# Optimization experiments

Measured on AMD Instinct MI355X. Metric: run time of the kernel, lower is better.

The kernel has to match this reference:

```python
import jax, jax.numpy as jnp
import numpy as np

B, N = 32, 512


def _stick_breaking(b, x_mask):
    """Row-major stick-breaking recurrence, O(N^2) sequential steps.

    Equivalent to the TF while_loop: for step in range(N*N), m=step//N, n=step%N:
      fut      = max(0, x_mask[:,m,n+1:] - sum_{m'<m} x[:,m',n+1:])  (col partial sums)
      mfm      = sum_j fut_j
      row_sum  = sum_{n'<n} x[:,m,n']
      col_sum  = sum_{m'<m} x[:,m',n]
      lower    = mask[m,n]*max(0, 1 - row_sum - mfm)
      upper    = mask[m,n]*min(1 - row_sum, 1 - col_sum)
      x[m,n]   = lower + b[m,n]*(upper - lower)
    Key insight: during row m the column partial sums are constant, so the
    future-mass terms for every n can be precomputed as an exclusive reverse
    cumsum; only the within-row dependency (row_sum) needs a scan.
    """
    Bb, Nn, _ = b.shape
    dt = b.dtype

    def row_step(col_sums, inputs):
        b_row, mask_row = inputs                      # [B, N] each
        fut = jnp.maximum(0.0, mask_row - col_sums)   # [B, N]
        # mfm[:, n] = sum_{j > n} fut[:, j]  (exclusive reverse cumsum)
        mfm = jnp.flip(jnp.cumsum(jnp.flip(fut, -1), axis=-1), -1) - fut

        def col_step(row_sum, inp):
            b_mn, m_mn, mfm_n, cs_n = inp             # [B] each
            lower = m_mn * jnp.maximum(0.0, 1.0 - row_sum - mfm_n)
            upper = m_mn * jnp.minimum(1.0 - row_sum, 1.0 - cs_n)
            p = lower + b_mn * (upper - lower)
            return row_sum + p, p

        _, row = jax.lax.scan(
            col_step,
            jnp.zeros((Bb,), dt),
            (b_row.T, mask_row.T, mfm.T, col_sums.T),
        )
        row = row.T                                   # [B, N]
        return col_sums + row, row

    _, rows = jax.lax.scan(
        row_step,
        jnp.zeros((Bb, Nn), dt),
        (jnp.swapaxes(b, 0, 1), jnp.swapaxes(x_mask, 0, 1)),
    )
    return jnp.swapaxes(rows, 0, 1)                   # [B, N, N]


def setup_inputs() -> dict:
    key = jax.random.key(0)
    k1, _ = jax.random.split(key)
    x = jax.random.normal(k1, (B, N, N), dtype=jnp.float32)
    x_mask = jnp.ones((B, N, N), dtype=jnp.float32)
    return {"x": x, "x_mask": x_mask}


def reference(x, x_mask):
    # layer.call applies sigmoid to the logits before stick-breaking
    return _stick_breaking(jax.nn.sigmoid(x), x_mask)
```

## Files before the change

kernel.cpp:

```cpp
#include <hip/hip_runtime.h>

#define NBATCH 32
#define NDIM 512
#define NFAST 448
#define NQUAD 112
#define NWAVE 8


__device__ __forceinline__ float prefix_inc(float x) {
  asm("s_nop 1\n\t"
      "v_add_f32_dpp %0, %0, %0 row_shr:1 row_mask:0xf bank_mask:0xf\n\t"
      "s_nop 1\n\t"
      "v_add_f32_dpp %0, %0, %0 row_shr:2 row_mask:0xf bank_mask:0xf\n\t"
      "s_nop 1\n\t"
      "v_add_f32_dpp %0, %0, %0 row_shr:4 row_mask:0xf bank_mask:0xf\n\t"
      "s_nop 1\n\t"
      "v_add_f32_dpp %0, %0, %0 row_shr:8 row_mask:0xf bank_mask:0xf\n\t"
      "s_nop 1\n\t"
      "v_add_f32_dpp %0, %0, %0 row_bcast:15 row_mask:0xa bank_mask:0xf\n\t"
      "s_nop 1\n\t"
      "v_add_f32_dpp %0, %0, %0 row_bcast:31 row_mask:0xc bank_mask:0xf\n\t"
      "s_nop 1"
      : "+v"(x));
  return x;
}

__device__ __forceinline__ void prefix_inc2(float& a, float& b) {
  asm("s_nop 1\n\t"
      "v_add_f32_dpp %0, %0, %0 row_shr:1 row_mask:0xf bank_mask:0xf\n\t"
      "v_add_f32_dpp %1, %1, %1 row_shr:1 row_mask:0xf bank_mask:0xf\n\t"
      "s_nop 0\n\t"
      "v_add_f32_dpp %0, %0, %0 row_shr:2 row_mask:0xf bank_mask:0xf\n\t"
      "v_add_f32_dpp %1, %1, %1 row_shr:2 row_mask:0xf bank_mask:0xf\n\t"
      "s_nop 0\n\t"
      "v_add_f32_dpp %0, %0, %0 row_shr:4 row_mask:0xf bank_mask:0xf\n\t"
      "v_add_f32_dpp %1, %1, %1 row_shr:4 row_mask:0xf bank_mask:0xf\n\t"
      "s_nop 0\n\t"
      "v_add_f32_dpp %0, %0, %0 row_shr:8 row_mask:0xf bank_mask:0xf\n\t"
      "v_add_f32_dpp %1, %1, %1 row_shr:8 row_mask:0xf bank_mask:0xf\n\t"
      "s_nop 0\n\t"
      "v_add_f32_dpp %0, %0, %0 row_bcast:15 row_mask:0xa bank_mask:0xf\n\t"
      "v_add_f32_dpp %1, %1, %1 row_bcast:15 row_mask:0xa bank_mask:0xf\n\t"
      "s_nop 0\n\t"
      "v_add_f32_dpp %0, %0, %0 row_bcast:31 row_mask:0xc bank_mask:0xf\n\t"
      "v_add_f32_dpp %1, %1, %1 row_bcast:31 row_mask:0xc bank_mask:0xf\n\t"
      "s_nop 1"
      : "+v"(a), "+v"(b));
}

__device__ __forceinline__ void aff_scan(float& A, float& B) {
  asm("s_nop 1\n\t"
      "v_fmac_f32_dpp %1, %1, %0 row_shr:1 row_mask:0xf bank_mask:0xf\n\t"
      "v_mul_f32_dpp  %0, %0, %0 row_shr:1 row_mask:0xf bank_mask:0xf\n\t"
      "s_nop 0\n\t"
      "v_fmac_f32_dpp %1, %1, %0 row_shr:2 row_mask:0xf bank_mask:0xf\n\t"
      "v_mul_f32_dpp  %0, %0, %0 row_shr:2 row_mask:0xf bank_mask:0xf\n\t"
      "s_nop 0\n\t"
      "v_fmac_f32_dpp %1, %1, %0 row_shr:4 row_mask:0xf bank_mask:0xf\n\t"
      "v_mul_f32_dpp  %0, %0, %0 row_shr:4 row_mask:0xf bank_mask:0xf\n\t"
      "s_nop 0\n\t"
      "v_fmac_f32_dpp %1, %1, %0 row_shr:8 row_mask:0xf bank_mask:0xf\n\t"
      "v_mul_f32_dpp  %0, %0, %0 row_shr:8 row_mask:0xf bank_mask:0xf\n\t"
      "s_nop 0\n\t"
      "v_fmac_f32_dpp %1, %1, %0 row_bcast:15 row_mask:0xa bank_mask:0xf\n\t"
      "v_mul_f32_dpp  %0, %0, %0 row_bcast:15 row_mask:0xa bank_mask:0xf\n\t"
      "s_nop 0\n\t"
      "v_fmac_f32_dpp %1, %1, %0 row_bcast:31 row_mask:0xc bank_mask:0xf\n\t"
      "v_mul_f32_dpp  %0, %0, %0 row_bcast:31 row_mask:0xc bank_mask:0xf\n\t"
      "s_nop 1"
      : "+v"(A), "+v"(B));
}

__device__ __forceinline__ float wave_shr1(float x, float fill) {
  return __int_as_float(__builtin_amdgcn_update_dpp(
      __float_as_int(fill), __float_as_int(x), 0x138 , 0xf, 0xf,
      false));
}

__device__ __forceinline__ void wg_barrier() {
  asm volatile("s_waitcnt lgkmcnt(0)" ::: "memory");
  __builtin_amdgcn_s_barrier();
  asm volatile("" ::: "memory");
}

__global__ __launch_bounds__(512, 2)
void sb_kernel(const float* __restrict__ x, const float* __restrict__ xm,
               float* __restrict__ out) {
  const int tid = (int)threadIdx.x;
  const int lane = tid & 63;
  const int w = __builtin_amdgcn_readfirstlane(tid >> 6);
  const int w2 = 2 * w;
  const size_t base =
      (size_t)blockIdx.x * NDIM * NDIM + (size_t)(w * 64 + lane);
  const float* xb = x + base;
  const float* mb = xm + base;
  float* ob = out + base;

  __shared__ float4 recs[NFAST];
  __shared__ alignas(16) float ex_sa[NWAVE];
  __shared__ alignas(16) float ex_S[NWAVE];
  __shared__ alignas(16) float ex_A[NWAVE];
  __shared__ alignas(16) float ex_B[NWAVE];

  float w8, t8;
  float c2_0, oc2_0, c2_1, oc2_1, c2_2, oc2_2, c2_3, oc2_3;
  float c1, c2, oc2;
  float fu = 0.0f, S = 0.0f;

  float X0 = xb[0], X1 = xb[NDIM], X2 = xb[2 * NDIM], X3 = xb[3 * NDIM];
  float M0 = mb[0], M1 = mb[NDIM], M2 = mb[2 * NDIM], M3 = mb[3 * NDIM];
  float Bx0 = xb[4 * NDIM], Bx1 = xb[5 * NDIM], Bx2 = xb[6 * NDIM],
        Bx3 = xb[7 * NDIM];
  float Bm0 = mb[4 * NDIM], Bm1 = mb[5 * NDIM], Bm2 = mb[6 * NDIM],
        Bm3 = mb[7 * NDIM];
  float Ax0 = Bx0, Ax1 = Bx1, Ax2 = Bx2, Ax3 = Bx3;
  float Am0 = Bm0, Am1 = Bm1, Am2 = Bm2, Am3 = Bm3;

  {
    float s0 = __builtin_amdgcn_rcpf(1.0f + __expf(-X0));
    float s1 = __builtin_amdgcn_rcpf(1.0f + __expf(-X1));
    float s2 = __builtin_amdgcn_rcpf(1.0f + __expf(-X2));
    float s3 = __builtin_amdgcn_rcpf(1.0f + __expf(-X3));
    c2_0 = M0 * s0;
    oc2_0 = 1.0f - c2_0;
    c2_1 = M1 * s1;
    oc2_1 = 1.0f - c2_1;
    c2_2 = M2 * s2;
    oc2_2 = 1.0f - c2_2;
    c2_3 = M3 * s3;
    oc2_3 = 1.0f - c2_3;
    w8 = 1.0f;
    t8 = c2_0;
  }

  const float* px = xb + (long)(8 - 8 * w) * NDIM;
  const float* pm = mb + (long)(8 - 8 * w) * NDIM;
  float* po = ob - (long)(8 * w) * NDIM;

  auto row_fast = [&](int m, const float4& r, float c2r, float oc2r,
                      float* pO) {
    float PA = prefix_inc(t8);
    float uin = fmaxf(1.0f - (r.z + (PA - t8)), 0.0f);
    bool pW = w8 < uin;
    float A = pW ? 1.0f : oc2r;
    float Bv = pW ? (-t8) : 0.0f;
    aff_scan(A, Bv);
    float Aex = wave_shr1(A, 1.0f);
    float Bex = wave_shr1(Bv, 0.0f);
    if (w < NWAVE - 1 && lane == 63)
      recs[m] = make_float4(A * r.x, fmaf(A, r.y, Bv), r.z + PA, 0.0f);
    float E = r.x + r.y;
    float e = fminf(fmaxf(fmaf(Aex, E, Bex), 0.0f), 1.0f);
    float p = c2r * fminf(e, w8);
    w8 -= p;
    *pO = p;
  };

  auto quad_step = [&](int t, int k, float& WX0, float& WX1, float& WX2,
                       float& WX3, float& WM0, float& WM1, float& WM2,
                       float& WM3, const float& RX0, const float& RX1,
                       const float& RX2, const float& RX3, const float& RM0,
                       const float& RM1, const float& RM2, const float& RM3) {
    const int q = t - w2;
    if ((unsigned)q < (unsigned)NQUAD) {
      const int m = 4 * q;
      float4 r0 = make_float4(1.0f, 0.0f, 0.0f, 0.0f);
      float4 r1 = r0, r2 = r0, r3 = r0;
      if (w > 0) {
        r0 = recs[m];
        r1 = recs[m + 1];
        r2 = recs[m + 2];
        r3 = recs[m + 3];
      }
      const float* pxk = px + (size_t)(4 * k) * NDIM;
      const float* pmk = pm + (size_t)(4 * k) * NDIM;
      WX0 = pxk[0];
      WX1 = pxk[NDIM];
      WX2 = pxk[2 * NDIM];
      WX3 = pxk[3 * NDIM];
      WM0 = pmk[0];
      WM1 = pmk[NDIM];
      WM2 = pmk[2 * NDIM];
      WM3 = pmk[3 * NDIM];

      float s0 = __builtin_amdgcn_rcpf(1.0f + __expf(-RX0));
      float s1 = __builtin_amdgcn_rcpf(1.0f + __expf(-RX1));
      float s2 = __builtin_amdgcn_rcpf(1.0f + __expf(-RX2));
      float s3 = __builtin_amdgcn_rcpf(1.0f + __expf(-RX3));
      float c2n0 = RM0 * s0, oc2n0 = 1.0f - c2n0;
      float c2n1 = RM1 * s1, oc2n1 = 1.0f - c2n1;
      float c2n2 = RM2 * s2, oc2n2 = 1.0f - c2n2;
      float c2n3 = RM3 * s3, oc2n3 = 1.0f - c2n3;

      float* pok = po + (size_t)(4 * k) * NDIM;
      row_fast(m + 0, r0, c2_0, oc2_0, pok);
      t8 = c2_1 * w8;
      row_fast(m + 1, r1, c2_1, oc2_1, pok + NDIM);
      t8 = c2_2 * w8;
      row_fast(m + 2, r2, c2_2, oc2_2, pok + 2 * NDIM);
      t8 = c2_3 * w8;
      row_fast(m + 3, r3, c2_3, oc2_3, pok + 3 * NDIM);
      t8 = c2n0 * w8;
      c2_0 = c2n0;
      oc2_0 = oc2n0;
      c2_1 = c2n1;
      oc2_1 = oc2n1;
      c2_2 = c2n2;
      oc2_2 = oc2n2;
      c2_3 = c2n3;
      oc2_3 = oc2n3;
    }
  };

#pragma unroll 1
  for (int t = 0; t < NQUAD + 2 * (NWAVE - 1); t += 2) {
    quad_step(t + 0, 0, Ax0, Ax1, Ax2, Ax3, Am0, Am1, Am2, Am3, Bx0, Bx1, Bx2,
              Bx3, Bm0, Bm1, Bm2, Bm3);
    quad_step(t + 1, 1, Bx0, Bx1, Bx2, Bx3, Bm0, Bm1, Bm2, Bm3, Ax0, Ax1, Ax2,
              Ax3, Am0, Am1, Am2, Am3);
    wg_barrier();
    px += 8 * NDIM;
    pm += 8 * NDIM;
    po += 8 * NDIM;
  }

  float fx0, fm0, fx1, fm1, fx2, fm2, fx3, fm3;
  {
    float m448 = mb[(size_t)448 * NDIM];
    fx1 = xb[(size_t)449 * NDIM];
    fm1 = mb[(size_t)449 * NDIM];
    fx2 = xb[(size_t)450 * NDIM];
    fm2 = mb[(size_t)450 * NDIM];
    fx3 = xb[(size_t)451 * NDIM];
    fm3 = mb[(size_t)451 * NDIM];
    fx0 = fx1;
    fm0 = fm1;
    c2 = c2_0;
    oc2 = oc2_0;
    c1 = m448 - c2;
    float om = 1.0f - m448;
    fu = fmaxf(w8 - om, 0.0f);
    S = fu;
  }

  auto row_full = [&](int m, float& WX, float& WM, const float& RX,
                      const float& RM) {
    const size_t nro = (size_t)((m + 4) & (NDIM - 1)) * NDIM;
    WX = xb[nro];
    WM = mb[nro];

    float PS = S, PA = t8;
    prefix_inc2(PS, PA);

    if (lane == 63) {
      ex_sa[w] = PA;
      ex_S[w] = PS;
    }
    wg_barrier();

    float4 sl = *(const float4*)&ex_sa[0];
    float4 sh = *(const float4*)&ex_sa[4];
    float4 Sl = *(const float4*)&ex_S[0];
    float4 Sh = *(const float4*)&ex_S[4];
    float off_sa = 0.0f, off_S = 0.0f;
    if (w > 0) { off_sa += sl.x; off_S += Sl.x; }
    if (w > 1) { off_sa += sl.y; off_S += Sl.y; }
    if (w > 2) { off_sa += sl.z; off_S += Sl.z; }
    if (w > 3) { off_sa += sl.w; off_S += Sl.w; }
    if (w > 4) { off_sa += sh.x; off_S += Sh.x; }
    if (w > 5) { off_sa += sh.y; off_S += Sh.y; }
    if (w > 6) { off_sa += sh.z; off_S += Sh.z; }
    float Tg =
        ((Sl.x + Sl.y) + (Sl.z + Sl.w)) + ((Sh.x + Sh.y) + (Sh.z + Sh.w));

    float uin = fmaxf(1.0f - (off_sa + (PA - t8)), 0.0f);
    float R_ = (Tg - off_S) - PS;
    float nc1m = -c1 * R_;

    bool pW = w8 < uin;
    float aP = pW ? 1.0f : oc2;
    float bP = pW ? (-t8) : 0.0f;
    bool pL = (uin - R_) > 0.0f;
    if (pL) {
      aP -= c1;
      bP -= nc1m;
    }

    float A = aP, Bv = bP;
    aff_scan(A, Bv);
    float Aex = wave_shr1(A, 1.0f);
    float Bex = wave_shr1(Bv, 0.0f);

    if (lane == 63) {
      ex_A[w] = A;
      ex_B[w] = Bv;
    }
    wg_barrier();

    float4 Al = *(const float4*)&ex_A[0];
    float4 Ah = *(const float4*)&ex_A[4];
    float4 Bl = *(const float4*)&ex_B[0];
    float4 Bh = *(const float4*)&ex_B[4];
    float E = 1.0f;
    if (w > 0) E = fmaf(Al.x, E, Bl.x);
    if (w > 1) E = fmaf(Al.y, E, Bl.y);
    if (w > 2) E = fmaf(Al.z, E, Bl.z);
    if (w > 3) E = fmaf(Al.w, E, Bl.w);
    if (w > 4) E = fmaf(Ah.x, E, Bh.x);
    if (w > 5) E = fmaf(Ah.y, E, Bh.y);
    if (w > 6) E = fmaf(Ah.z, E, Bh.z);
    float e = fminf(fmaxf(fmaf(Aex, E, Bex), 0.0f), 1.0f);

    float sg = __builtin_amdgcn_rcpf(1.0f + __expf(-RX));
    float c2n = RM * sg;
    float oc2n = 1.0f - c2n;
    float c1n = RM - c2n;
    float omn = 1.0f - RM;

    float U = fminf(e, w8);
    float g = fmaxf(fmaf(c1, e, nc1m), 0.0f);
    float p = fmaf(c2, U, g);
    w8 -= p;
    ob[(size_t)m * NDIM] = p;

    t8 = c2n * w8;
    fu = fmaxf(w8 - omn, 0.0f);
    S = fu;
    c2 = c2n;
    oc2 = oc2n;
    c1 = c1n;
  };

#pragma unroll 1
  for (int m = NFAST; m < NDIM; m += 4) {
    row_full(m + 0, fx0, fm0, fx1, fm1);
    row_full(m + 1, fx1, fm1, fx2, fm2);
    row_full(m + 2, fx2, fm2, fx3, fm3);
    row_full(m + 3, fx3, fm3, fx0, fm0);
  }
}

extern "C" void kernel_launch(void* const* d_in, const int* in_sizes, int n_in,
                              void* d_out, int out_size, void* d_ws,
                              size_t ws_size, hipStream_t stream) {
  const float* x = (const float*)d_in[0];
  const float* xmask = (const float*)d_in[1];
  float* out = (float*)d_out;
  (void)in_sizes;
  (void)n_in;
  (void)out_size;
  (void)d_ws;
  (void)ws_size;
  hipLaunchKernelGGL(sb_kernel, dim3(NBATCH), dim3(512), 0, stream, x, xmask,
                     out);
}
```

Before: 235.6 us.

## Tighten wave pipeline skew to one quad and hide sigmoid in DPP scan nops

Cuts the skew of the wavefront pipeline across waves from two quads to one and puts a barrier after every quad step instead of every pair, so the loop has fewer fill steps. The sigmoid for the next rows is now computed inside the inline-asm DPP prefix scan, filling the s_nop slots that were previously idle. The cost is twice as many workgroup barriers, plus hand-scheduled asm whose hazard spacing must stay correct for DPP. Prefetch register setup is adjusted to match the new skew.

```diff
diff --git a/kernel.cpp b/kernel.cpp
--- a/kernel.cpp
+++ b/kernel.cpp
@@ -7,22 +7,29 @@
 #define NWAVE 8
 
 
-__device__ __forceinline__ float prefix_inc(float x) {
-  asm("s_nop 1\n\t"
+__device__ __forceinline__ void prefix_prep(float& p, float rx, float rm,
+                                            float& c2n, float& oc2n) {
+  float t0, t1, t2;
+  asm("v_mul_f32 %1, 0xbfb8aa3b, %6\n\t"
+      "s_nop 0\n\t"
       "v_add_f32_dpp %0, %0, %0 row_shr:1 row_mask:0xf bank_mask:0xf\n\t"
-      "s_nop 1\n\t"
+      "v_exp_f32 %1, %1\n\t"
+      "s_nop 0\n\t"
       "v_add_f32_dpp %0, %0, %0 row_shr:2 row_mask:0xf bank_mask:0xf\n\t"
-      "s_nop 1\n\t"
+      "v_add_f32 %2, 1.0, %1\n\t"
+      "s_nop 0\n\t"
       "v_add_f32_dpp %0, %0, %0 row_shr:4 row_mask:0xf bank_mask:0xf\n\t"
-      "s_nop 1\n\t"
+      "v_rcp_f32 %3, %2\n\t"
+      "s_nop 0\n\t"
       "v_add_f32_dpp %0, %0, %0 row_shr:8 row_mask:0xf bank_mask:0xf\n\t"
-      "s_nop 1\n\t"
+      "v_mul_f32 %4, %7, %3\n\t"
+      "s_nop 0\n\t"
       "v_add_f32_dpp %0, %0, %0 row_bcast:15 row_mask:0xa bank_mask:0xf\n\t"
-      "s_nop 1\n\t"
-      "v_add_f32_dpp %0, %0, %0 row_bcast:31 row_mask:0xc bank_mask:0xf\n\t"
-      "s_nop 1"
-      : "+v"(x));
-  return x;
+      "v_sub_f32 %5, 1.0, %4\n\t"
+      "s_nop 0\n\t"
+      "v_add_f32_dpp %0, %0, %0 row_bcast:31 row_mask:0xc bank_mask:0xf"
+      : "+v"(p), "=&v"(t0), "=&v"(t1), "=&v"(t2), "=&v"(c2n), "=&v"(oc2n)
+      : "v"(rx), "v"(rm));
 }
 
 __device__ __forceinline__ void prefix_inc2(float& a, float& b) {
@@ -89,7 +96,6 @@
   const int tid = (int)threadIdx.x;
   const int lane = tid & 63;
   const int w = __builtin_amdgcn_readfirstlane(tid >> 6);
-  const int w2 = 2 * w;
   const size_t base =
       (size_t)blockIdx.x * NDIM * NDIM + (size_t)(w * 64 + lane);
   const float* xb = x + base;
@@ -109,12 +115,14 @@
 
   float X0 = xb[0], X1 = xb[NDIM], X2 = xb[2 * NDIM], X3 = xb[3 * NDIM];
   float M0 = mb[0], M1 = mb[NDIM], M2 = mb[2 * NDIM], M3 = mb[3 * NDIM];
-  float Bx0 = xb[4 * NDIM], Bx1 = xb[5 * NDIM], Bx2 = xb[6 * NDIM],
-        Bx3 = xb[7 * NDIM];
-  float Bm0 = mb[4 * NDIM], Bm1 = mb[5 * NDIM], Bm2 = mb[6 * NDIM],
-        Bm3 = mb[7 * NDIM];
-  float Ax0 = Bx0, Ax1 = Bx1, Ax2 = Bx2, Ax3 = Bx3;
-  float Am0 = Bm0, Am1 = Bm1, Am2 = Bm2, Am3 = Bm3;
+  float q1x0 = xb[4 * NDIM], q1x1 = xb[5 * NDIM], q1x2 = xb[6 * NDIM],
+        q1x3 = xb[7 * NDIM];
+  float q1m0 = mb[4 * NDIM], q1m1 = mb[5 * NDIM], q1m2 = mb[6 * NDIM],
+        q1m3 = mb[7 * NDIM];
+  float Ax0 = q1x0, Ax1 = q1x1, Ax2 = q1x2, Ax3 = q1x3;
+  float Am0 = q1m0, Am1 = q1m1, Am2 = q1m2, Am3 = q1m3;
+  float Bx0 = q1x0, Bx1 = q1x1, Bx2 = q1x2, Bx3 = q1x3;
+  float Bm0 = q1m0, Bm1 = q1m1, Bm2 = q1m2, Bm3 = q1m3;
 
   {
     float s0 = __builtin_amdgcn_rcpf(1.0f + __expf(-X0));
@@ -133,13 +141,15 @@
     t8 = c2_0;
   }
 
-  const float* px = xb + (long)(8 - 8 * w) * NDIM;
-  const float* pm = mb + (long)(8 - 8 * w) * NDIM;
-  float* po = ob - (long)(8 * w) * NDIM;
+  const float* px = xb + (long)(8 - 4 * w) * NDIM;
+  const float* pm = mb + (long)(8 - 4 * w) * NDIM;
+  float* po = ob - (long)(4 * w) * NDIM;
 
   auto row_fast = [&](int m, const float4& r, float c2r, float oc2r,
+                      float rx, float rm, float& c2n, float& oc2n,
                       float* pO) {
-    float PA = prefix_inc(t8);
+    float PA = t8;
+    prefix_prep(PA, rx, rm, c2n, oc2n);
     float uin = fmaxf(1.0f - (r.z + (PA - t8)), 0.0f);
     bool pW = w8 < uin;
     float A = pW ? 1.0f : oc2r;
@@ -161,7 +171,7 @@
                        float& WM3, const float& RX0, const float& RX1,
                        const float& RX2, const float& RX3, const float& RM0,
                        const float& RM1, const float& RM2, const float& RM3) {
-    const int q = t - w2;
+    const int q = t - w;
     if ((unsigned)q < (unsigned)NQUAD) {
       const int m = 4 * q;
       float4 r0 = make_float4(1.0f, 0.0f, 0.0f, 0.0f);
@@ -183,23 +193,17 @@
       WM2 = pmk[2 * NDIM];
       WM3 = pmk[3 * NDIM];
 
-      float s0 = __builtin_amdgcn_rcpf(1.0f + __expf(-RX0));
-      float s1 = __builtin_amdgcn_rcpf(1.0f + __expf(-RX1));
-      float s2 = __builtin_amdgcn_rcpf(1.0f + __expf(-RX2));
-      float s3 = __builtin_amdgcn_rcpf(1.0f + __expf(-RX3));
-      float c2n0 = RM0 * s0, oc2n0 = 1.0f - c2n0;
-      float c2n1 = RM1 * s1, oc2n1 = 1.0f - c2n1;
-      float c2n2 = RM2 * s2, oc2n2 = 1.0f - c2n2;
-      float c2n3 = RM3 * s3, oc2n3 = 1.0f - c2n3;
-
+      float c2n0, oc2n0, c2n1, oc2n1, c2n2, oc2n2, c2n3, oc2n3;
       float* pok = po + (size_t)(4 * k) * NDIM;
-      row_fast(m + 0, r0, c2_0, oc2_0, pok);
+      row_fast(m + 0, r0, c2_0, oc2_0, RX0, RM0, c2n0, oc2n0, pok);
       t8 = c2_1 * w8;
-      row_fast(m + 1, r1, c2_1, oc2_1, pok + NDIM);
+      row_fast(m + 1, r1, c2_1, oc2_1, RX1, RM1, c2n1, oc2n1, pok + NDIM);
       t8 = c2_2 * w8;
-      row_fast(m + 2, r2, c2_2, oc2_2, pok + 2 * NDIM);
+      row_fast(m + 2, r2, c2_2, oc2_2, RX2, RM2, c2n2, oc2n2,
+               pok + 2 * NDIM);
       t8 = c2_3 * w8;
-      row_fast(m + 3, r3, c2_3, oc2_3, pok + 3 * NDIM);
+      row_fast(m + 3, r3, c2_3, oc2_3, RX3, RM3, c2n3, oc2n3,
+               pok + 3 * NDIM);
       t8 = c2n0 * w8;
       c2_0 = c2n0;
       oc2_0 = oc2n0;
@@ -210,15 +214,15 @@
       c2_3 = c2n3;
       oc2_3 = oc2n3;
     }
+    wg_barrier();
   };
 
 #pragma unroll 1
-  for (int t = 0; t < NQUAD + 2 * (NWAVE - 1); t += 2) {
+  for (int t = 0; t < NQUAD + NWAVE; t += 2) {
     quad_step(t + 0, 0, Ax0, Ax1, Ax2, Ax3, Am0, Am1, Am2, Am3, Bx0, Bx1, Bx2,
               Bx3, Bm0, Bm1, Bm2, Bm3);
     quad_step(t + 1, 1, Bx0, Bx1, Bx2, Bx3, Bm0, Bm1, Bm2, Bm3, Ax0, Ax1, Ax2,
               Ax3, Am0, Am1, Am2, Am3);
-    wg_barrier();
     px += 8 * NDIM;
     pm += 8 * NDIM;
     po += 8 * NDIM;
```

After: 236.4 us. No clear change (+0.3%).
